# Kernel tuning notes

Hardware: AMD Instinct MI355X
Metric: run time of the kernel (lower is better)

Reference implementation:

```python
import jax, jax.numpy as jnp
import numpy as np

EPS = 1e-6
SMOOTH = 0.025


def setup_inputs() -> dict:
    key = jax.random.key(0)
    k1, = jax.random.split(key, 1)
    x = jax.random.uniform(k1, (32, 128, 8000), dtype=jnp.float32)  # (B, C, T) energies >= 0
    alpha = jnp.float32(0.98)
    delta = jnp.float32(2.0)
    r = jnp.float32(0.5)
    return {"x": x, "alpha": alpha, "delta": delta, "r": r}


def reference(x, alpha, delta, r):
    # x: (B, C, T)
    x = jnp.maximum(x, 0.0)
    xt = jnp.moveaxis(x, -1, 0)  # (T, B, C) for time scan

    def ema_step(M, xt_t):
        M = (1.0 - SMOOTH) * M + SMOOTH * xt_t
        return M, M

    M0 = jnp.zeros(x.shape[:2], dtype=x.dtype)  # (B, C)
    _, Mt = jax.lax.scan(ema_step, M0, xt)  # (T, B, C)
    M = jnp.moveaxis(Mt, 0, -1)  # (B, C, T)

    norm = x / jnp.power(EPS + M, alpha)
    y = jnp.power(norm + delta, r) - jnp.power(delta, r)
    return y
```

## Files before the change

### kernel.cpp

```cpp
#include <hip/hip_runtime.h>

#define EPSV   1e-6f
#define SMOOTH 0.025f
#define HALF   4096
#define WARM   512

typedef float v4f __attribute__((ext_vector_type(4)));

__device__ __forceinline__ float fast_log2(float v) { return __builtin_amdgcn_logf(v); }
__device__ __forceinline__ float fast_exp2(float v) { return __builtin_amdgcn_exp2f(v); }

__device__ __forceinline__ float pcen_elem(float xr, float M, float nalpha,
                                           float delta, float r, float dr) {
    float m    = EPSV + M;
    float norm = xr * fast_exp2(nalpha * fast_log2(m));
    return fast_exp2(r * fast_log2(norm + delta)) - dr;
}

struct KC {
    float a1, a2, a3, a4;
    float e0, e1, e2, e3, e4, e5;
    float a4lane;
    float a256;
    int   lane;
};

__device__ __forceinline__ void scan_group(const KC& c,
                                           const float xa[4], const float xb[4],
                                           float& m0, float Ma[4], float Mb[4]) {
    const float b = SMOOTH;
    float qa0 = b * xa[0];
    float qa1 = fmaf(c.a1, qa0, b * xa[1]);
    float qa2 = fmaf(c.a1, qa1, b * xa[2]);
    float qa3 = fmaf(c.a1, qa2, b * xa[3]);
    float qb0 = b * xb[0];
    float qb1 = fmaf(c.a1, qb0, b * xb[1]);
    float qb2 = fmaf(c.a1, qb1, b * xb[2]);
    float qb3 = fmaf(c.a1, qb2, b * xb[3]);

    float PA = qa3, PB = qb3, u;
    u = __shfl_up(PA, 1, 64);  PA = fmaf(c.lane >= 1  ? c.e0 : 0.f, u, PA);
    u = __shfl_up(PB, 1, 64);  PB = fmaf(c.lane >= 1  ? c.e0 : 0.f, u, PB);
    u = __shfl_up(PA, 2, 64);  PA = fmaf(c.lane >= 2  ? c.e1 : 0.f, u, PA);
    u = __shfl_up(PB, 2, 64);  PB = fmaf(c.lane >= 2  ? c.e1 : 0.f, u, PB);
    u = __shfl_up(PA, 4, 64);  PA = fmaf(c.lane >= 4  ? c.e2 : 0.f, u, PA);
    u = __shfl_up(PB, 4, 64);  PB = fmaf(c.lane >= 4  ? c.e2 : 0.f, u, PB);
    u = __shfl_up(PA, 8, 64);  PA = fmaf(c.lane >= 8  ? c.e3 : 0.f, u, PA);
    u = __shfl_up(PB, 8, 64);  PB = fmaf(c.lane >= 8  ? c.e3 : 0.f, u, PB);
    u = __shfl_up(PA, 16, 64); PA = fmaf(c.lane >= 16 ? c.e4 : 0.f, u, PA);
    u = __shfl_up(PB, 16, 64); PB = fmaf(c.lane >= 16 ? c.e4 : 0.f, u, PB);
    u = __shfl_up(PA, 32, 64); PA = fmaf(c.lane >= 32 ? c.e5 : 0.f, u, PA);
    u = __shfl_up(PB, 32, 64); PB = fmaf(c.lane >= 32 ? c.e5 : 0.f, u, PB);

    float TA = __shfl(PA, 63, 64);
    float TB = __shfl(PB, 63, 64);
    float PexcA = __shfl_up(PA, 1, 64); if (c.lane == 0) PexcA = 0.f;
    float PexcB = __shfl_up(PB, 1, 64); if (c.lane == 0) PexcB = 0.f;

    float mA = m0;
    float mB = fmaf(c.a256, m0, TA);
    m0       = fmaf(c.a256, mB, TB);

    float sA = fmaf(c.a4lane, mA, PexcA);
    float sB = fmaf(c.a4lane, mB, PexcB);
    Ma[0] = fmaf(c.a1, sA, qa0);
    Ma[1] = fmaf(c.a2, sA, qa1);
    Ma[2] = fmaf(c.a3, sA, qa2);
    Ma[3] = fmaf(c.a4, sA, qa3);
    Mb[0] = fmaf(c.a1, sB, qb0);
    Mb[1] = fmaf(c.a2, sB, qb1);
    Mb[2] = fmaf(c.a3, sB, qb2);
    Mb[3] = fmaf(c.a4, sB, qb3);
}

__global__ __launch_bounds__(256, 6) void pcen_ema_kernel(
    const float* __restrict__ x,
    const float* __restrict__ alpha_p,
    const float* __restrict__ delta_p,
    const float* __restrict__ r_p,
    float* __restrict__ y,
    int rows, int T)
{
    const int gid   = blockIdx.x * blockDim.x + threadIdx.x;
    const int wave  = gid >> 6;
    const int lane  = gid & 63;
    const int row   = wave >> 1;
    const int chunk = wave & 1;
    if (row >= rows) return;

    const float nalpha = -alpha_p[0];
    const float delta  = delta_p[0];
    const float r      = r_p[0];
    const float dr     = fast_exp2(r * fast_log2(delta));

    KC c;
    c.lane = lane;
    const float a = 1.0f - SMOOTH;
    c.a1 = a;  c.a2 = a * a;  c.a3 = c.a2 * a;  c.a4 = c.a2 * c.a2;
    c.e0 = c.a4;      c.e1 = c.e0 * c.e0;  c.e2 = c.e1 * c.e1;
    c.e3 = c.e2 * c.e2; c.e4 = c.e3 * c.e3; c.e5 = c.e4 * c.e4;
    c.a256 = c.e5 * c.e5;
    float a4l = 1.0f;
    if (lane & 1)  a4l *= c.e0;
    if (lane & 2)  a4l *= c.e1;
    if (lane & 4)  a4l *= c.e2;
    if (lane & 8)  a4l *= c.e3;
    if (lane & 16) a4l *= c.e4;
    if (lane & 32) a4l *= c.e5;
    c.a4lane = a4l;

    const long long base = (long long)row * T;
    const float* __restrict__ xrow = x + base;
    float* __restrict__       yrow = y + base;

    const int tstart = chunk ? HALF : 0;
    const int tend   = chunk ? T    : HALF;
    const int off    = 4 * lane;

    float m0 = 0.0f;

    if (chunk) {
        const int tw = HALF - WARM;
        v4f wa = *(const v4f*)(xrow + tw + off);
        v4f wb = *(const v4f*)(xrow + tw + 256 + off);
        float xa[4] = { fmaxf(wa.x,0.f), fmaxf(wa.y,0.f), fmaxf(wa.z,0.f), fmaxf(wa.w,0.f) };
        float xb[4] = { fmaxf(wb.x,0.f), fmaxf(wb.y,0.f), fmaxf(wb.z,0.f), fmaxf(wb.w,0.f) };
        float Ma[4], Mb[4];
        scan_group(c, xa, xb, m0, Ma, Mb);
    }

    const int nfull = (tend - tstart) >> 9;
    int t = tstart;

    v4f va = {0,0,0,0}, vb = va;
    if (nfull > 0) {
        va = *(const v4f*)(xrow + t + off);
        vb = *(const v4f*)(xrow + t + 256 + off);
    }
    for (int i = 0; i < nfull; ++i) {
        const int tn = t + 512;
        const int tp = (i + 1 < nfull) ? tn : t;
        v4f na = *(const v4f*)(xrow + tp + off);
        v4f nb = *(const v4f*)(xrow + tp + 256 + off);

        float xa[4] = { fmaxf(va.x,0.f), fmaxf(va.y,0.f), fmaxf(va.z,0.f), fmaxf(va.w,0.f) };
        float xb[4] = { fmaxf(vb.x,0.f), fmaxf(vb.y,0.f), fmaxf(vb.z,0.f), fmaxf(vb.w,0.f) };
        float Ma[4], Mb[4];
        scan_group(c, xa, xb, m0, Ma, Mb);

        v4f oa, ob;
        oa.x = pcen_elem(xa[0], Ma[0], nalpha, delta, r, dr);
        oa.y = pcen_elem(xa[1], Ma[1], nalpha, delta, r, dr);
        oa.z = pcen_elem(xa[2], Ma[2], nalpha, delta, r, dr);
        oa.w = pcen_elem(xa[3], Ma[3], nalpha, delta, r, dr);
        ob.x = pcen_elem(xb[0], Mb[0], nalpha, delta, r, dr);
        ob.y = pcen_elem(xb[1], Mb[1], nalpha, delta, r, dr);
        ob.z = pcen_elem(xb[2], Mb[2], nalpha, delta, r, dr);
        ob.w = pcen_elem(xb[3], Mb[3], nalpha, delta, r, dr);
        __builtin_nontemporal_store(oa, (v4f*)(yrow + t + off));
        __builtin_nontemporal_store(ob, (v4f*)(yrow + t + 256 + off));

        va = na; vb = nb; t = tn;
    }

    if (t < tend) {
        float xa[4], xb[4];
        #pragma unroll
        for (int k = 0; k < 4; ++k) {
            int ia = t + off + k;
            int ib = t + 256 + off + k;
            xa[k] = (ia < tend) ? fmaxf(xrow[ia], 0.f) : 0.f;
            xb[k] = (ib < tend) ? fmaxf(xrow[ib], 0.f) : 0.f;
        }
        float Ma[4], Mb[4];
        scan_group(c, xa, xb, m0, Ma, Mb);
        #pragma unroll
        for (int k = 0; k < 4; ++k) {
            int ia = t + off + k;
            int ib = t + 256 + off + k;
            if (ia < tend) yrow[ia] = pcen_elem(xa[k], Ma[k], nalpha, delta, r, dr);
            if (ib < tend) yrow[ib] = pcen_elem(xb[k], Mb[k], nalpha, delta, r, dr);
        }
    }
}

extern "C" void kernel_launch(void* const* d_in, const int* in_sizes, int n_in,
                              void* d_out, int out_size, void* d_ws, size_t ws_size,
                              hipStream_t stream) {
    const float* x     = (const float*)d_in[0];
    const float* alpha = (const float*)d_in[1];
    const float* delta = (const float*)d_in[2];
    const float* r     = (const float*)d_in[3];
    float* y = (float*)d_out;

    const int T     = 8000;
    const int total = in_sizes[0];
    const int rows  = total / T;

    const int waves   = rows * 2;
    const int threads = waves * 64;
    const int block   = 256;
    const int grid    = (threads + block - 1) / block;
    pcen_ema_kernel<<<grid, block, 0, stream>>>(x, alpha, delta, r, y, rows, T);
}
```

Baseline: 46.92 us.

## Split each row's scan into four chunks and specialize sqrt for r=0.5

Each row's time scan is now split into four chunks of 2000 samples instead of two halves, and the launch creates four waves per row. This raises parallelism (16384 waves) and shortens each wave's serial chain. Chunks after the first warm up their state on the preceding 512 samples, so redundant warm-up work grows. The power with exponent r is replaced by sqrt when r equals 0.5 at runtime, and the launch-bounds occupancy hint is raised. Chunk boundaries at 2000 are not multiples of 512, so the tail path now runs in every chunk and the vector loads may be misaligned.

```diff
diff --git a/kernel.cpp b/kernel.cpp
--- a/kernel.cpp
+++ b/kernel.cpp
@@ -2,20 +2,13 @@
 
 #define EPSV   1e-6f
 #define SMOOTH 0.025f
-#define HALF   4096
+#define NCHUNK 4
 #define WARM   512
 
 typedef float v4f __attribute__((ext_vector_type(4)));
 
 __device__ __forceinline__ float fast_log2(float v) { return __builtin_amdgcn_logf(v); }
 __device__ __forceinline__ float fast_exp2(float v) { return __builtin_amdgcn_exp2f(v); }
-
-__device__ __forceinline__ float pcen_elem(float xr, float M, float nalpha,
-                                           float delta, float r, float dr) {
-    float m    = EPSV + M;
-    float norm = xr * fast_exp2(nalpha * fast_log2(m));
-    return fast_exp2(r * fast_log2(norm + delta)) - dr;
-}
 
 struct KC {
     float a1, a2, a3, a4;
@@ -73,7 +66,12 @@
     Mb[3] = fmaf(c.a4, sB, qb3);
 }
 
-__global__ __launch_bounds__(256, 6) void pcen_ema_kernel(
+__device__ __forceinline__ float pcen_norm(float xr, float M, float nalpha, float delta) {
+    float m = EPSV + M;
+    return fmaf(xr, fast_exp2(nalpha * fast_log2(m)), delta);
+}
+
+__global__ __launch_bounds__(256, 16) void pcen_ema_kernel(
     const float* __restrict__ x,
     const float* __restrict__ alpha_p,
     const float* __restrict__ delta_p,
@@ -84,21 +82,23 @@
     const int gid   = blockIdx.x * blockDim.x + threadIdx.x;
     const int wave  = gid >> 6;
     const int lane  = gid & 63;
-    const int row   = wave >> 1;
-    const int chunk = wave & 1;
+    const int row   = wave >> 2;
+    const int chunk = wave & 3;
     if (row >= rows) return;
 
     const float nalpha = -alpha_p[0];
     const float delta  = delta_p[0];
     const float r      = r_p[0];
-    const float dr     = fast_exp2(r * fast_log2(delta));
+    const bool  rhalf  = (r == 0.5f);
+    const float dr     = rhalf ? __builtin_sqrtf(delta)
+                               : fast_exp2(r * fast_log2(delta));
 
     KC c;
     c.lane = lane;
     const float a = 1.0f - SMOOTH;
     c.a1 = a;  c.a2 = a * a;  c.a3 = c.a2 * a;  c.a4 = c.a2 * c.a2;
-    c.e0 = c.a4;      c.e1 = c.e0 * c.e0;  c.e2 = c.e1 * c.e1;
-    c.e3 = c.e2 * c.e2; c.e4 = c.e3 * c.e3; c.e5 = c.e4 * c.e4;
+    c.e0 = c.a4;        c.e1 = c.e0 * c.e0;  c.e2 = c.e1 * c.e1;
+    c.e3 = c.e2 * c.e2; c.e4 = c.e3 * c.e3;  c.e5 = c.e4 * c.e4;
     c.a256 = c.e5 * c.e5;
     float a4l = 1.0f;
     if (lane & 1)  a4l *= c.e0;
@@ -113,14 +113,15 @@
     const float* __restrict__ xrow = x + base;
     float* __restrict__       yrow = y + base;
 
-    const int tstart = chunk ? HALF : 0;
-    const int tend   = chunk ? T    : HALF;
+    const int csz    = T / NCHUNK;
+    const int tstart = chunk * csz;
+    const int tend   = tstart + csz;
     const int off    = 4 * lane;
 
     float m0 = 0.0f;
 
-    if (chunk) {
-        const int tw = HALF - WARM;
+    if (chunk != 0) {
+        const int tw = tstart - WARM;
         v4f wa = *(const v4f*)(xrow + tw + off);
         v4f wb = *(const v4f*)(xrow + tw + 256 + off);
         float xa[4] = { fmaxf(wa.x,0.f), fmaxf(wa.y,0.f), fmaxf(wa.z,0.f), fmaxf(wa.w,0.f) };
@@ -148,15 +149,32 @@
         float Ma[4], Mb[4];
         scan_group(c, xa, xb, m0, Ma, Mb);
 
+        float na_[4], nb_[4];
+        #pragma unroll
+        for (int k = 0; k < 4; ++k) na_[k] = pcen_norm(xa[k], Ma[k], nalpha, delta);
+        #pragma unroll
+        for (int k = 0; k < 4; ++k) nb_[k] = pcen_norm(xb[k], Mb[k], nalpha, delta);
+
         v4f oa, ob;
-        oa.x = pcen_elem(xa[0], Ma[0], nalpha, delta, r, dr);
-        oa.y = pcen_elem(xa[1], Ma[1], nalpha, delta, r, dr);
-        oa.z = pcen_elem(xa[2], Ma[2], nalpha, delta, r, dr);
-        oa.w = pcen_elem(xa[3], Ma[3], nalpha, delta, r, dr);
-        ob.x = pcen_elem(xb[0], Mb[0], nalpha, delta, r, dr);
-        ob.y = pcen_elem(xb[1], Mb[1], nalpha, delta, r, dr);
-        ob.z = pcen_elem(xb[2], Mb[2], nalpha, delta, r, dr);
-        ob.w = pcen_elem(xb[3], Mb[3], nalpha, delta, r, dr);
+        if (rhalf) {
+            oa.x = __builtin_sqrtf(na_[0]) - dr;
+            oa.y = __builtin_sqrtf(na_[1]) - dr;
+            oa.z = __builtin_sqrtf(na_[2]) - dr;
+            oa.w = __builtin_sqrtf(na_[3]) - dr;
+            ob.x = __builtin_sqrtf(nb_[0]) - dr;
+            ob.y = __builtin_sqrtf(nb_[1]) - dr;
+            ob.z = __builtin_sqrtf(nb_[2]) - dr;
+            ob.w = __builtin_sqrtf(nb_[3]) - dr;
+        } else {
+            oa.x = fast_exp2(r * fast_log2(na_[0])) - dr;
+            oa.y = fast_exp2(r * fast_log2(na_[1])) - dr;
+            oa.z = fast_exp2(r * fast_log2(na_[2])) - dr;
+            oa.w = fast_exp2(r * fast_log2(na_[3])) - dr;
+            ob.x = fast_exp2(r * fast_log2(nb_[0])) - dr;
+            ob.y = fast_exp2(r * fast_log2(nb_[1])) - dr;
+            ob.z = fast_exp2(r * fast_log2(nb_[2])) - dr;
+            ob.w = fast_exp2(r * fast_log2(nb_[3])) - dr;
+        }
         __builtin_nontemporal_store(oa, (v4f*)(yrow + t + off));
         __builtin_nontemporal_store(ob, (v4f*)(yrow + t + 256 + off));
 
@@ -178,8 +196,16 @@
         for (int k = 0; k < 4; ++k) {
             int ia = t + off + k;
             int ib = t + 256 + off + k;
-            if (ia < tend) yrow[ia] = pcen_elem(xa[k], Ma[k], nalpha, delta, r, dr);
-            if (ib < tend) yrow[ib] = pcen_elem(xb[k], Mb[k], nalpha, delta, r, dr);
+            if (ia < tend) {
+                float n = pcen_norm(xa[k], Ma[k], nalpha, delta);
+                yrow[ia] = (rhalf ? __builtin_sqrtf(n)
+                                  : fast_exp2(r * fast_log2(n))) - dr;
+            }
+            if (ib < tend) {
+                float n = pcen_norm(xb[k], Mb[k], nalpha, delta);
+                yrow[ib] = (rhalf ? __builtin_sqrtf(n)
+                                  : fast_exp2(r * fast_log2(n))) - dr;
+            }
         }
     }
 }
@@ -197,7 +223,7 @@
     const int total = in_sizes[0];
     const int rows  = total / T;
 
-    const int waves   = rows * 2;
+    const int waves   = rows * NCHUNK;
     const int threads = waves * 64;
     const int block   = 256;
     const int grid    = (threads + block - 1) / block;
```

Result: slower. 53.66 us (+14.4%).

## Process four interleaved 256-element scan groups per iteration and specialize sqrt for r=0.5

Applied to the files above, without the earlier changes.

The time loop now handles 1024 elements per iteration as four independent intra-wave scans whose shuffle steps are interleaved. This gives more instruction-level parallelism and halves the number of serialized loop iterations and carry steps. Tail handling moves into the main loop through clamped loads and guarded stores. A runtime check for r == 0.5 replaces the exp2/log2 power with sqrt, with the general path kept. Launch bounds rise to 8 waves per SIMD, which may add register pressure from the wider unroll.

```diff
diff --git a/kernel.cpp b/kernel.cpp
--- a/kernel.cpp
+++ b/kernel.cpp
@@ -9,13 +9,6 @@
 
 __device__ __forceinline__ float fast_log2(float v) { return __builtin_amdgcn_logf(v); }
 __device__ __forceinline__ float fast_exp2(float v) { return __builtin_amdgcn_exp2f(v); }
-
-__device__ __forceinline__ float pcen_elem(float xr, float M, float nalpha,
-                                           float delta, float r, float dr) {
-    float m    = EPSV + M;
-    float norm = xr * fast_exp2(nalpha * fast_log2(m));
-    return fast_exp2(r * fast_log2(norm + delta)) - dr;
-}
 
 struct KC {
     float a1, a2, a3, a4;
@@ -25,9 +18,69 @@
     int   lane;
 };
 
-__device__ __forceinline__ void scan_group(const KC& c,
-                                           const float xa[4], const float xb[4],
-                                           float& m0, float Ma[4], float Mb[4]) {
+#define KS_STEP(P, d, e) \
+    u = __shfl_up(P, d, 64); P = fmaf(c.lane >= d ? e : 0.f, u, P);
+
+__device__ __forceinline__ void scan4(const KC& c,
+        const float x0[4], const float x1[4], const float x2[4], const float x3[4],
+        float& m0, float M0[4], float M1[4], float M2[4], float M3[4]) {
+    const float b = SMOOTH;
+    float q00 = b * x0[0];
+    float q01 = fmaf(c.a1, q00, b * x0[1]);
+    float q02 = fmaf(c.a1, q01, b * x0[2]);
+    float q03 = fmaf(c.a1, q02, b * x0[3]);
+    float q10 = b * x1[0];
+    float q11 = fmaf(c.a1, q10, b * x1[1]);
+    float q12 = fmaf(c.a1, q11, b * x1[2]);
+    float q13 = fmaf(c.a1, q12, b * x1[3]);
+    float q20 = b * x2[0];
+    float q21 = fmaf(c.a1, q20, b * x2[1]);
+    float q22 = fmaf(c.a1, q21, b * x2[2]);
+    float q23 = fmaf(c.a1, q22, b * x2[3]);
+    float q30 = b * x3[0];
+    float q31 = fmaf(c.a1, q30, b * x3[1]);
+    float q32 = fmaf(c.a1, q31, b * x3[2]);
+    float q33 = fmaf(c.a1, q32, b * x3[3]);
+
+    float P0 = q03, P1 = q13, P2 = q23, P3 = q33, u;
+    KS_STEP(P0, 1,  c.e0) KS_STEP(P1, 1,  c.e0) KS_STEP(P2, 1,  c.e0) KS_STEP(P3, 1,  c.e0)
+    KS_STEP(P0, 2,  c.e1) KS_STEP(P1, 2,  c.e1) KS_STEP(P2, 2,  c.e1) KS_STEP(P3, 2,  c.e1)
+    KS_STEP(P0, 4,  c.e2) KS_STEP(P1, 4,  c.e2) KS_STEP(P2, 4,  c.e2) KS_STEP(P3, 4,  c.e2)
+    KS_STEP(P0, 8,  c.e3) KS_STEP(P1, 8,  c.e3) KS_STEP(P2, 8,  c.e3) KS_STEP(P3, 8,  c.e3)
+    KS_STEP(P0, 16, c.e4) KS_STEP(P1, 16, c.e4) KS_STEP(P2, 16, c.e4) KS_STEP(P3, 16, c.e4)
+    KS_STEP(P0, 32, c.e5) KS_STEP(P1, 32, c.e5) KS_STEP(P2, 32, c.e5) KS_STEP(P3, 32, c.e5)
+
+    float T0 = __shfl(P0, 63, 64);
+    float T1 = __shfl(P1, 63, 64);
+    float T2 = __shfl(P2, 63, 64);
+    float T3 = __shfl(P3, 63, 64);
+    float E0 = __shfl_up(P0, 1, 64); if (c.lane == 0) E0 = 0.f;
+    float E1 = __shfl_up(P1, 1, 64); if (c.lane == 0) E1 = 0.f;
+    float E2 = __shfl_up(P2, 1, 64); if (c.lane == 0) E2 = 0.f;
+    float E3 = __shfl_up(P3, 1, 64); if (c.lane == 0) E3 = 0.f;
+
+    float mA = m0;
+    float mB = fmaf(c.a256, mA, T0);
+    float mC = fmaf(c.a256, mB, T1);
+    float mD = fmaf(c.a256, mC, T2);
+    m0       = fmaf(c.a256, mD, T3);
+
+    float s0 = fmaf(c.a4lane, mA, E0);
+    float s1 = fmaf(c.a4lane, mB, E1);
+    float s2 = fmaf(c.a4lane, mC, E2);
+    float s3 = fmaf(c.a4lane, mD, E3);
+    M0[0] = fmaf(c.a1, s0, q00); M0[1] = fmaf(c.a2, s0, q01);
+    M0[2] = fmaf(c.a3, s0, q02); M0[3] = fmaf(c.a4, s0, q03);
+    M1[0] = fmaf(c.a1, s1, q10); M1[1] = fmaf(c.a2, s1, q11);
+    M1[2] = fmaf(c.a3, s1, q12); M1[3] = fmaf(c.a4, s1, q13);
+    M2[0] = fmaf(c.a1, s2, q20); M2[1] = fmaf(c.a2, s2, q21);
+    M2[2] = fmaf(c.a3, s2, q22); M2[3] = fmaf(c.a4, s2, q23);
+    M3[0] = fmaf(c.a1, s3, q30); M3[1] = fmaf(c.a2, s3, q31);
+    M3[2] = fmaf(c.a3, s3, q32); M3[3] = fmaf(c.a4, s3, q33);
+}
+
+__device__ __forceinline__ void scan2(const KC& c,
+        const float xa[4], const float xb[4], float& m0) {
     const float b = SMOOTH;
     float qa0 = b * xa[0];
     float qa1 = fmaf(c.a1, qa0, b * xa[1]);
@@ -39,41 +92,25 @@
     float qb3 = fmaf(c.a1, qb2, b * xb[3]);
 
     float PA = qa3, PB = qb3, u;
-    u = __shfl_up(PA, 1, 64);  PA = fmaf(c.lane >= 1  ? c.e0 : 0.f, u, PA);
-    u = __shfl_up(PB, 1, 64);  PB = fmaf(c.lane >= 1  ? c.e0 : 0.f, u, PB);
-    u = __shfl_up(PA, 2, 64);  PA = fmaf(c.lane >= 2  ? c.e1 : 0.f, u, PA);
-    u = __shfl_up(PB, 2, 64);  PB = fmaf(c.lane >= 2  ? c.e1 : 0.f, u, PB);
-    u = __shfl_up(PA, 4, 64);  PA = fmaf(c.lane >= 4  ? c.e2 : 0.f, u, PA);
-    u = __shfl_up(PB, 4, 64);  PB = fmaf(c.lane >= 4  ? c.e2 : 0.f, u, PB);
-    u = __shfl_up(PA, 8, 64);  PA = fmaf(c.lane >= 8  ? c.e3 : 0.f, u, PA);
-    u = __shfl_up(PB, 8, 64);  PB = fmaf(c.lane >= 8  ? c.e3 : 0.f, u, PB);
-    u = __shfl_up(PA, 16, 64); PA = fmaf(c.lane >= 16 ? c.e4 : 0.f, u, PA);
-    u = __shfl_up(PB, 16, 64); PB = fmaf(c.lane >= 16 ? c.e4 : 0.f, u, PB);
-    u = __shfl_up(PA, 32, 64); PA = fmaf(c.lane >= 32 ? c.e5 : 0.f, u, PA);
-    u = __shfl_up(PB, 32, 64); PB = fmaf(c.lane >= 32 ? c.e5 : 0.f, u, PB);
+    KS_STEP(PA, 1,  c.e0) KS_STEP(PB, 1,  c.e0)
+    KS_STEP(PA, 2,  c.e1) KS_STEP(PB, 2,  c.e1)
+    KS_STEP(PA, 4,  c.e2) KS_STEP(PB, 4,  c.e2)
+    KS_STEP(PA, 8,  c.e3) KS_STEP(PB, 8,  c.e3)
+    KS_STEP(PA, 16, c.e4) KS_STEP(PB, 16, c.e4)
+    KS_STEP(PA, 32, c.e5) KS_STEP(PB, 32, c.e5)
 
     float TA = __shfl(PA, 63, 64);
     float TB = __shfl(PB, 63, 64);
-    float PexcA = __shfl_up(PA, 1, 64); if (c.lane == 0) PexcA = 0.f;
-    float PexcB = __shfl_up(PB, 1, 64); if (c.lane == 0) PexcB = 0.f;
-
-    float mA = m0;
     float mB = fmaf(c.a256, m0, TA);
     m0       = fmaf(c.a256, mB, TB);
-
-    float sA = fmaf(c.a4lane, mA, PexcA);
-    float sB = fmaf(c.a4lane, mB, PexcB);
-    Ma[0] = fmaf(c.a1, sA, qa0);
-    Ma[1] = fmaf(c.a2, sA, qa1);
-    Ma[2] = fmaf(c.a3, sA, qa2);
-    Ma[3] = fmaf(c.a4, sA, qa3);
-    Mb[0] = fmaf(c.a1, sB, qb0);
-    Mb[1] = fmaf(c.a2, sB, qb1);
-    Mb[2] = fmaf(c.a3, sB, qb2);
-    Mb[3] = fmaf(c.a4, sB, qb3);
-}
-
-__global__ __launch_bounds__(256, 6) void pcen_ema_kernel(
+}
+
+__device__ __forceinline__ float pcen_norm(float xr, float M, float nalpha, float delta) {
+    float m = EPSV + M;
+    return fmaf(xr, fast_exp2(nalpha * fast_log2(m)), delta);
+}
+
+__global__ __launch_bounds__(256, 8) void pcen_ema_kernel(
     const float* __restrict__ x,
     const float* __restrict__ alpha_p,
     const float* __restrict__ delta_p,
@@ -91,14 +128,16 @@
     const float nalpha = -alpha_p[0];
     const float delta  = delta_p[0];
     const float r      = r_p[0];
-    const float dr     = fast_exp2(r * fast_log2(delta));
+    const bool  rhalf  = (r == 0.5f);
+    const float dr     = rhalf ? __builtin_sqrtf(delta)
+                               : fast_exp2(r * fast_log2(delta));
 
     KC c;
     c.lane = lane;
     const float a = 1.0f - SMOOTH;
     c.a1 = a;  c.a2 = a * a;  c.a3 = c.a2 * a;  c.a4 = c.a2 * c.a2;
-    c.e0 = c.a4;      c.e1 = c.e0 * c.e0;  c.e2 = c.e1 * c.e1;
-    c.e3 = c.e2 * c.e2; c.e4 = c.e3 * c.e3; c.e5 = c.e4 * c.e4;
+    c.e0 = c.a4;        c.e1 = c.e0 * c.e0;  c.e2 = c.e1 * c.e1;
+    c.e3 = c.e2 * c.e2; c.e4 = c.e3 * c.e3;  c.e5 = c.e4 * c.e4;
     c.a256 = c.e5 * c.e5;
     float a4l = 1.0f;
     if (lane & 1)  a4l *= c.e0;
@@ -125,62 +164,82 @@
         v4f wb = *(const v4f*)(xrow + tw + 256 + off);
         float xa[4] = { fmaxf(wa.x,0.f), fmaxf(wa.y,0.f), fmaxf(wa.z,0.f), fmaxf(wa.w,0.f) };
         float xb[4] = { fmaxf(wb.x,0.f), fmaxf(wb.y,0.f), fmaxf(wb.z,0.f), fmaxf(wb.w,0.f) };
-        float Ma[4], Mb[4];
-        scan_group(c, xa, xb, m0, Ma, Mb);
+        scan2(c, xa, xb, m0);
     }
 
-    const int nfull = (tend - tstart) >> 9;
+    const int span  = tend - tstart;
+    const int ngrp  = (span + 1023) >> 10;
     int t = tstart;
 
-    v4f va = {0,0,0,0}, vb = va;
-    if (nfull > 0) {
-        va = *(const v4f*)(xrow + t + off);
-        vb = *(const v4f*)(xrow + t + 256 + off);
+    v4f v0, v1, v2, v3;
+    {
+        const int lim = tend - 4;
+        int t0 = t + off, t1 = t + 256 + off, t2 = t + 512 + off, t3 = t + 768 + off;
+        v0 = *(const v4f*)(xrow + (t0 < lim ? t0 : lim));
+        v1 = *(const v4f*)(xrow + (t1 < lim ? t1 : lim));
+        v2 = *(const v4f*)(xrow + (t2 < lim ? t2 : lim));
+        v3 = *(const v4f*)(xrow + (t3 < lim ? t3 : lim));
     }
-    for (int i = 0; i < nfull; ++i) {
-        const int tn = t + 512;
-        const int tp = (i + 1 < nfull) ? tn : t;
-        v4f na = *(const v4f*)(xrow + tp + off);
-        v4f nb = *(const v4f*)(xrow + tp + 256 + off);
-
-        float xa[4] = { fmaxf(va.x,0.f), fmaxf(va.y,0.f), fmaxf(va.z,0.f), fmaxf(va.w,0.f) };
-        float xb[4] = { fmaxf(vb.x,0.f), fmaxf(vb.y,0.f), fmaxf(vb.z,0.f), fmaxf(vb.w,0.f) };
-        float Ma[4], Mb[4];
-        scan_group(c, xa, xb, m0, Ma, Mb);
-
-        v4f oa, ob;
-        oa.x = pcen_elem(xa[0], Ma[0], nalpha, delta, r, dr);
-        oa.y = pcen_elem(xa[1], Ma[1], nalpha, delta, r, dr);
-        oa.z = pcen_elem(xa[2], Ma[2], nalpha, delta, r, dr);
-        oa.w = pcen_elem(xa[3], Ma[3], nalpha, delta, r, dr);
-        ob.x = pcen_elem(xb[0], Mb[0], nalpha, delta, r, dr);
-        ob.y = pcen_elem(xb[1], Mb[1], nalpha, delta, r, dr);
-        ob.z = pcen_elem(xb[2], Mb[2], nalpha, delta, r, dr);
-        ob.w = pcen_elem(xb[3], Mb[3], nalpha, delta, r, dr);
-        __builtin_nontemporal_store(oa, (v4f*)(yrow + t + off));
-        __builtin_nontemporal_store(ob, (v4f*)(yrow + t + 256 + off));
-
-        va = na; vb = nb; t = tn;
-    }
-
-    if (t < tend) {
-        float xa[4], xb[4];
+    for (int i = 0; i < ngrp; ++i) {
+        const int tn = t + 1024;
+        v4f n0, n1, n2, n3;
+        {
+            const int tb  = (i + 1 < ngrp) ? tn : t;
+            const int lim = tend - 4;
+            int t0 = tb + off, t1 = tb + 256 + off, t2 = tb + 512 + off, t3 = tb + 768 + off;
+            n0 = *(const v4f*)(xrow + (t0 < lim ? t0 : lim));
+            n1 = *(const v4f*)(xrow + (t1 < lim ? t1 : lim));
+            n2 = *(const v4f*)(xrow + (t2 < lim ? t2 : lim));
+            n3 = *(const v4f*)(xrow + (t3 < lim ? t3 : lim));
+        }
+
+        float x0[4] = { fmaxf(v0.x,0.f), fmaxf(v0.y,0.f), fmaxf(v0.z,0.f), fmaxf(v0.w,0.f) };
+        float x1[4] = { fmaxf(v1.x,0.f), fmaxf(v1.y,0.f), fmaxf(v1.z,0.f), fmaxf(v1.w,0.f) };
+        float x2[4] = { fmaxf(v2.x,0.f), fmaxf(v2.y,0.f), fmaxf(v2.z,0.f), fmaxf(v2.w,0.f) };
+        float x3[4] = { fmaxf(v3.x,0.f), fmaxf(v3.y,0.f), fmaxf(v3.z,0.f), fmaxf(v3.w,0.f) };
+        float M0[4], M1[4], M2[4], M3[4];
+        scan4(c, x0, x1, x2, x3, m0, M0, M1, M2, M3);
+
+        float p0[4], p1[4], p2[4], p3[4];
         #pragma unroll
         for (int k = 0; k < 4; ++k) {
-            int ia = t + off + k;
-            int ib = t + 256 + off + k;
-            xa[k] = (ia < tend) ? fmaxf(xrow[ia], 0.f) : 0.f;
-            xb[k] = (ib < tend) ? fmaxf(xrow[ib], 0.f) : 0.f;
-        }
-        float Ma[4], Mb[4];
-        scan_group(c, xa, xb, m0, Ma, Mb);
-        #pragma unroll
-        for (int k = 0; k < 4; ++k) {
-            int ia = t + off + k;
-            int ib = t + 256 + off + k;
-            if (ia < tend) yrow[ia] = pcen_elem(xa[k], Ma[k], nalpha, delta, r, dr);
-            if (ib < tend) yrow[ib] = pcen_elem(xb[k], Mb[k], nalpha, delta, r, dr);
-        }
+            p0[k] = pcen_norm(x0[k], M0[k], nalpha, delta);
+            p1[k] = pcen_norm(x1[k], M1[k], nalpha, delta);
+            p2[k] = pcen_norm(x2[k], M2[k], nalpha, delta);
+            p3[k] = pcen_norm(x3[k], M3[k], nalpha, delta);
+        }
+
+        v4f o0, o1, o2, o3;
+        if (rhalf) {
+            #pragma unroll
+            for (int k = 0; k < 4; ++k) {
+                ((float*)&o0)[k] = __builtin_sqrtf(p0[k]) - dr;
+                ((float*)&o1)[k] = __builtin_sqrtf(p1[k]) - dr;
+                ((float*)&o2)[k] = __builtin_sqrtf(p2[k]) - dr;
+                ((float*)&o3)[k] = __builtin_sqrtf(p3[k]) - dr;
+            }
+        } else {
+            #pragma unroll
+            for (int k = 0; k < 4; ++k) {
+                ((float*)&o0)[k] = fast_exp2(r * fast_log2(p0[k])) - dr;
+                ((float*)&o1)[k] = fast_exp2(r * fast_log2(p1[k])) - dr;
+                ((float*)&o2)[k] = fast_exp2(r * fast_log2(p2[k])) - dr;
+                ((float*)&o3)[k] = fast_exp2(r * fast_log2(p3[k])) - dr;
+            }
+        }
+        if (tn <= tend) {
+            __builtin_nontemporal_store(o0, (v4f*)(yrow + t + off));
+            __builtin_nontemporal_store(o1, (v4f*)(yrow + t + 256 + off));
+            __builtin_nontemporal_store(o2, (v4f*)(yrow + t + 512 + off));
+            __builtin_nontemporal_store(o3, (v4f*)(yrow + t + 768 + off));
+        } else {
+            if (t + off       + 4 <= tend) __builtin_nontemporal_store(o0, (v4f*)(yrow + t + off));
+            if (t + 256 + off + 4 <= tend) __builtin_nontemporal_store(o1, (v4f*)(yrow + t + 256 + off));
+            if (t + 512 + off + 4 <= tend) __builtin_nontemporal_store(o2, (v4f*)(yrow + t + 512 + off));
+            if (t + 768 + off + 4 <= tend) __builtin_nontemporal_store(o3, (v4f*)(yrow + t + 768 + off));
+        }
+
+        v0 = n0; v1 = n1; v2 = n2; v3 = n3; t = tn;
     }
 }
 
```

After: 94.33 us. 101% more time.

## Deepen prefetch to two groups, specialize r=0.5 with sqrt, merge tail into loop

Applied to the files above, without the earlier changes.

Prefetching now runs two 512-element groups ahead instead of one, so more loads are in flight while the serial scan runs. Loads are clamped to stay in bounds, which lets the scalar tail path fold into the main loop with guarded vector stores. When r equals 0.5, a sqrt replaces the exp2/log2 pair, and the per-lane shuffle masks are precomputed once. The deeper prefetch raises register pressure, and the tail stores assume the remaining length is a multiple of 4.

```diff
diff --git a/kernel.cpp b/kernel.cpp
--- a/kernel.cpp
+++ b/kernel.cpp
@@ -10,20 +10,17 @@
 __device__ __forceinline__ float fast_log2(float v) { return __builtin_amdgcn_logf(v); }
 __device__ __forceinline__ float fast_exp2(float v) { return __builtin_amdgcn_exp2f(v); }
 
-__device__ __forceinline__ float pcen_elem(float xr, float M, float nalpha,
-                                           float delta, float r, float dr) {
-    float m    = EPSV + M;
-    float norm = xr * fast_exp2(nalpha * fast_log2(m));
-    return fast_exp2(r * fast_log2(norm + delta)) - dr;
-}
-
 struct KC {
     float a1, a2, a3, a4;
-    float e0, e1, e2, e3, e4, e5;
+    float e0m, e1m, e2m, e3m, e4m, e5m;
     float a4lane;
     float a256;
     int   lane;
 };
+
+#define KS2(PA, PB, d, em) \
+    uA = __shfl_up(PA, d, 64); uB = __shfl_up(PB, d, 64); \
+    PA = fmaf(em, uA, PA);     PB = fmaf(em, uB, PB);
 
 __device__ __forceinline__ void scan_group(const KC& c,
                                            const float xa[4], const float xb[4],
@@ -38,39 +35,34 @@
     float qb2 = fmaf(c.a1, qb1, b * xb[2]);
     float qb3 = fmaf(c.a1, qb2, b * xb[3]);
 
-    float PA = qa3, PB = qb3, u;
-    u = __shfl_up(PA, 1, 64);  PA = fmaf(c.lane >= 1  ? c.e0 : 0.f, u, PA);
-    u = __shfl_up(PB, 1, 64);  PB = fmaf(c.lane >= 1  ? c.e0 : 0.f, u, PB);
-    u = __shfl_up(PA, 2, 64);  PA = fmaf(c.lane >= 2  ? c.e1 : 0.f, u, PA);
-    u = __shfl_up(PB, 2, 64);  PB = fmaf(c.lane >= 2  ? c.e1 : 0.f, u, PB);
-    u = __shfl_up(PA, 4, 64);  PA = fmaf(c.lane >= 4  ? c.e2 : 0.f, u, PA);
-    u = __shfl_up(PB, 4, 64);  PB = fmaf(c.lane >= 4  ? c.e2 : 0.f, u, PB);
-    u = __shfl_up(PA, 8, 64);  PA = fmaf(c.lane >= 8  ? c.e3 : 0.f, u, PA);
-    u = __shfl_up(PB, 8, 64);  PB = fmaf(c.lane >= 8  ? c.e3 : 0.f, u, PB);
-    u = __shfl_up(PA, 16, 64); PA = fmaf(c.lane >= 16 ? c.e4 : 0.f, u, PA);
-    u = __shfl_up(PB, 16, 64); PB = fmaf(c.lane >= 16 ? c.e4 : 0.f, u, PB);
-    u = __shfl_up(PA, 32, 64); PA = fmaf(c.lane >= 32 ? c.e5 : 0.f, u, PA);
-    u = __shfl_up(PB, 32, 64); PB = fmaf(c.lane >= 32 ? c.e5 : 0.f, u, PB);
+    float PA = qa3, PB = qb3, uA, uB;
+    KS2(PA, PB, 1,  c.e0m)
+    KS2(PA, PB, 2,  c.e1m)
+    KS2(PA, PB, 4,  c.e2m)
+    KS2(PA, PB, 8,  c.e3m)
+    KS2(PA, PB, 16, c.e4m)
+    KS2(PA, PB, 32, c.e5m)
 
     float TA = __shfl(PA, 63, 64);
     float TB = __shfl(PB, 63, 64);
-    float PexcA = __shfl_up(PA, 1, 64); if (c.lane == 0) PexcA = 0.f;
-    float PexcB = __shfl_up(PB, 1, 64); if (c.lane == 0) PexcB = 0.f;
+    float EA = __shfl_up(PA, 1, 64); if (c.lane == 0) EA = 0.f;
+    float EB = __shfl_up(PB, 1, 64); if (c.lane == 0) EB = 0.f;
 
     float mA = m0;
-    float mB = fmaf(c.a256, m0, TA);
+    float mB = fmaf(c.a256, mA, TA);
     m0       = fmaf(c.a256, mB, TB);
 
-    float sA = fmaf(c.a4lane, mA, PexcA);
-    float sB = fmaf(c.a4lane, mB, PexcB);
-    Ma[0] = fmaf(c.a1, sA, qa0);
-    Ma[1] = fmaf(c.a2, sA, qa1);
-    Ma[2] = fmaf(c.a3, sA, qa2);
-    Ma[3] = fmaf(c.a4, sA, qa3);
-    Mb[0] = fmaf(c.a1, sB, qb0);
-    Mb[1] = fmaf(c.a2, sB, qb1);
-    Mb[2] = fmaf(c.a3, sB, qb2);
-    Mb[3] = fmaf(c.a4, sB, qb3);
+    float sA = fmaf(c.a4lane, mA, EA);
+    float sB = fmaf(c.a4lane, mB, EB);
+    Ma[0] = fmaf(c.a1, sA, qa0); Ma[1] = fmaf(c.a2, sA, qa1);
+    Ma[2] = fmaf(c.a3, sA, qa2); Ma[3] = fmaf(c.a4, sA, qa3);
+    Mb[0] = fmaf(c.a1, sB, qb0); Mb[1] = fmaf(c.a2, sB, qb1);
+    Mb[2] = fmaf(c.a3, sB, qb2); Mb[3] = fmaf(c.a4, sB, qb3);
+}
+
+__device__ __forceinline__ float pcen_norm(float xr, float M, float nalpha, float delta) {
+    float m = EPSV + M;
+    return fmaf(xr, fast_exp2(nalpha * fast_log2(m)), delta);
 }
 
 __global__ __launch_bounds__(256, 6) void pcen_ema_kernel(
@@ -91,22 +83,31 @@
     const float nalpha = -alpha_p[0];
     const float delta  = delta_p[0];
     const float r      = r_p[0];
-    const float dr     = fast_exp2(r * fast_log2(delta));
+    const bool  rhalf  = (r == 0.5f);
+    const float dr     = rhalf ? __builtin_sqrtf(delta)
+                               : fast_exp2(r * fast_log2(delta));
 
     KC c;
     c.lane = lane;
     const float a = 1.0f - SMOOTH;
     c.a1 = a;  c.a2 = a * a;  c.a3 = c.a2 * a;  c.a4 = c.a2 * c.a2;
-    c.e0 = c.a4;      c.e1 = c.e0 * c.e0;  c.e2 = c.e1 * c.e1;
-    c.e3 = c.e2 * c.e2; c.e4 = c.e3 * c.e3; c.e5 = c.e4 * c.e4;
-    c.a256 = c.e5 * c.e5;
+    const float e0 = c.a4;       const float e1 = e0 * e0;
+    const float e2 = e1 * e1;    const float e3 = e2 * e2;
+    const float e4 = e3 * e3;    const float e5 = e4 * e4;
+    c.a256 = e5 * e5;
+    c.e0m = lane >= 1  ? e0 : 0.f;
+    c.e1m = lane >= 2  ? e1 : 0.f;
+    c.e2m = lane >= 4  ? e2 : 0.f;
+    c.e3m = lane >= 8  ? e3 : 0.f;
+    c.e4m = lane >= 16 ? e4 : 0.f;
+    c.e5m = lane >= 32 ? e5 : 0.f;
     float a4l = 1.0f;
-    if (lane & 1)  a4l *= c.e0;
-    if (lane & 2)  a4l *= c.e1;
-    if (lane & 4)  a4l *= c.e2;
-    if (lane & 8)  a4l *= c.e3;
-    if (lane & 16) a4l *= c.e4;
-    if (lane & 32) a4l *= c.e5;
+    if (lane & 1)  a4l *= e0;
+    if (lane & 2)  a4l *= e1;
+    if (lane & 4)  a4l *= e2;
+    if (lane & 8)  a4l *= e3;
+    if (lane & 16) a4l *= e4;
+    if (lane & 32) a4l *= e5;
     c.a4lane = a4l;
 
     const long long base = (long long)row * T;
@@ -116,6 +117,7 @@
     const int tstart = chunk ? HALF : 0;
     const int tend   = chunk ? T    : HALF;
     const int off    = 4 * lane;
+    const int lim    = tend - 4;
 
     float m0 = 0.0f;
 
@@ -125,62 +127,70 @@
         v4f wb = *(const v4f*)(xrow + tw + 256 + off);
         float xa[4] = { fmaxf(wa.x,0.f), fmaxf(wa.y,0.f), fmaxf(wa.z,0.f), fmaxf(wa.w,0.f) };
         float xb[4] = { fmaxf(wb.x,0.f), fmaxf(wb.y,0.f), fmaxf(wb.z,0.f), fmaxf(wb.w,0.f) };
-        float Ma[4], Mb[4];
-        scan_group(c, xa, xb, m0, Ma, Mb);
+        float Md[4], Me[4];
+        scan_group(c, xa, xb, m0, Md, Me);
     }
 
-    const int nfull = (tend - tstart) >> 9;
+    const int ngrp = ((tend - tstart) + 511) >> 9;
     int t = tstart;
 
-    v4f va = {0,0,0,0}, vb = va;
-    if (nfull > 0) {
-        va = *(const v4f*)(xrow + t + off);
-        vb = *(const v4f*)(xrow + t + 256 + off);
+    v4f va, vb, wa, wb;
+    {
+        int p0 = t + off,        p1 = t + 256 + off;
+        va = *(const v4f*)(xrow + (p0 < lim ? p0 : lim));
+        vb = *(const v4f*)(xrow + (p1 < lim ? p1 : lim));
+        int p2 = t + 512 + off,  p3 = t + 768 + off;
+        wa = *(const v4f*)(xrow + (p2 < lim ? p2 : lim));
+        wb = *(const v4f*)(xrow + (p3 < lim ? p3 : lim));
     }
-    for (int i = 0; i < nfull; ++i) {
+
+    for (int i = 0; i < ngrp; ++i) {
         const int tn = t + 512;
-        const int tp = (i + 1 < nfull) ? tn : t;
-        v4f na = *(const v4f*)(xrow + tp + off);
-        v4f nb = *(const v4f*)(xrow + tp + 256 + off);
+        const int tp = (i + 2 < ngrp) ? t + 1024 : t;
+        int p0 = tp + off, p1 = tp + 256 + off;
+        v4f za = *(const v4f*)(xrow + (p0 < lim ? p0 : lim));
+        v4f zb = *(const v4f*)(xrow + (p1 < lim ? p1 : lim));
 
         float xa[4] = { fmaxf(va.x,0.f), fmaxf(va.y,0.f), fmaxf(va.z,0.f), fmaxf(va.w,0.f) };
         float xb[4] = { fmaxf(vb.x,0.f), fmaxf(vb.y,0.f), fmaxf(vb.z,0.f), fmaxf(vb.w,0.f) };
         float Ma[4], Mb[4];
         scan_group(c, xa, xb, m0, Ma, Mb);
 
+        float pa0 = pcen_norm(xa[0], Ma[0], nalpha, delta);
+        float pa1 = pcen_norm(xa[1], Ma[1], nalpha, delta);
+        float pa2 = pcen_norm(xa[2], Ma[2], nalpha, delta);
+        float pa3 = pcen_norm(xa[3], Ma[3], nalpha, delta);
+        float pb0 = pcen_norm(xb[0], Mb[0], nalpha, delta);
+        float pb1 = pcen_norm(xb[1], Mb[1], nalpha, delta);
+        float pb2 = pcen_norm(xb[2], Mb[2], nalpha, delta);
+        float pb3 = pcen_norm(xb[3], Mb[3], nalpha, delta);
+
         v4f oa, ob;
-        oa.x = pcen_elem(xa[0], Ma[0], nalpha, delta, r, dr);
-        oa.y = pcen_elem(xa[1], Ma[1], nalpha, delta, r, dr);
-        oa.z = pcen_elem(xa[2], Ma[2], nalpha, delta, r, dr);
-        oa.w = pcen_elem(xa[3], Ma[3], nalpha, delta, r, dr);
-        ob.x = pcen_elem(xb[0], Mb[0], nalpha, delta, r, dr);
-        ob.y = pcen_elem(xb[1], Mb[1], nalpha, delta, r, dr);
-        ob.z = pcen_elem(xb[2], Mb[2], nalpha, delta, r, dr);
-        ob.w = pcen_elem(xb[3], Mb[3], nalpha, delta, r, dr);
-        __builtin_nontemporal_store(oa, (v4f*)(yrow + t + off));
-        __builtin_nontemporal_store(ob, (v4f*)(yrow + t + 256 + off));
-
-        va = na; vb = nb; t = tn;
-    }
-
-    if (t < tend) {
-        float xa[4], xb[4];
-        #pragma unroll
-        for (int k = 0; k < 4; ++k) {
-            int ia = t + off + k;
-            int ib = t + 256 + off + k;
-            xa[k] = (ia < tend) ? fmaxf(xrow[ia], 0.f) : 0.f;
-            xb[k] = (ib < tend) ? fmaxf(xrow[ib], 0.f) : 0.f;
+        if (rhalf) {
+            oa.x = __builtin_sqrtf(pa0) - dr; oa.y = __builtin_sqrtf(pa1) - dr;
+            oa.z = __builtin_sqrtf(pa2) - dr; oa.w = __builtin_sqrtf(pa3) - dr;
+            ob.x = __builtin_sqrtf(pb0) - dr; ob.y = __builtin_sqrtf(pb1) - dr;
+            ob.z = __builtin_sqrtf(pb2) - dr; ob.w = __builtin_sqrtf(pb3) - dr;
+        } else {
+            oa.x = fast_exp2(r * fast_log2(pa0)) - dr;
+            oa.y = fast_exp2(r * fast_log2(pa1)) - dr;
+            oa.z = fast_exp2(r * fast_log2(pa2)) - dr;
+            oa.w = fast_exp2(r * fast_log2(pa3)) - dr;
+            ob.x = fast_exp2(r * fast_log2(pb0)) - dr;
+            ob.y = fast_exp2(r * fast_log2(pb1)) - dr;
+            ob.z = fast_exp2(r * fast_log2(pb2)) - dr;
+            ob.w = fast_exp2(r * fast_log2(pb3)) - dr;
         }
-        float Ma[4], Mb[4];
-        scan_group(c, xa, xb, m0, Ma, Mb);
-        #pragma unroll
-        for (int k = 0; k < 4; ++k) {
-            int ia = t + off + k;
-            int ib = t + 256 + off + k;
-            if (ia < tend) yrow[ia] = pcen_elem(xa[k], Ma[k], nalpha, delta, r, dr);
-            if (ib < tend) yrow[ib] = pcen_elem(xb[k], Mb[k], nalpha, delta, r, dr);
+
+        if (tn <= tend) {
+            __builtin_nontemporal_store(oa, (v4f*)(yrow + t + off));
+            __builtin_nontemporal_store(ob, (v4f*)(yrow + t + 256 + off));
+        } else {
+            if (t + off       + 4 <= tend) __builtin_nontemporal_store(oa, (v4f*)(yrow + t + off));
+            if (t + 256 + off + 4 <= tend) __builtin_nontemporal_store(ob, (v4f*)(yrow + t + 256 + off));
         }
+
+        va = wa; vb = wb; wa = za; wb = zb; t = tn;
     }
 }
 
```

After: 50.53 us. 7.7% more time.
